# Performance work log

Measured on AMD Instinct MI355X. Metric: run time of the kernel, lower is better.

Reference implementation:

```python
import jax, jax.numpy as jnp
import numpy as np

D_MODEL = 1024
D_STATE = 16
D_CONV = 4
EXPAND = 2
D_INNER = EXPAND * D_MODEL          # 2048
DT_RANK = D_MODEL // 16             # 64
BATCH, SEQ = 4, 2048


def setup_inputs() -> dict:
    key = jax.random.key(0)
    ks = jax.random.split(key, 8)
    s = lambda k, shape, sc=0.02: jax.random.normal(k, shape, jnp.float32) * sc
    x = jax.random.normal(ks[0], (BATCH, SEQ, D_MODEL), jnp.float32)
    tau = jax.random.uniform(ks[1], (BATCH, SEQ), jnp.float32) * 7200.0  # seconds
    # S4D-real init for A
    A_log = jnp.log(jnp.broadcast_to(jnp.arange(1, D_STATE + 1, dtype=jnp.float32), (D_INNER, D_STATE)))
    return dict(
        x=x, tau=tau,
        ln_g=jnp.ones((D_MODEL,), jnp.float32),
        ln_b=jnp.zeros((D_MODEL,), jnp.float32),
        in_proj_w=s(ks[2], (2 * D_INNER, D_MODEL)),
        conv_w=s(ks[3], (D_INNER, 1, D_CONV), 0.1),   # depthwise [O, I/g=1, K]
        conv_b=jnp.zeros((D_INNER,), jnp.float32),
        x_proj_w=s(ks[4], (DT_RANK + 2 * D_STATE, D_INNER)),
        dt_proj_w=s(ks[5], (D_INNER, DT_RANK), 0.1),
        dt_proj_b=jnp.full((D_INNER,), -4.6, jnp.float32),  # softplus ~ 0.01
        A_log=A_log,
        D=jnp.ones((D_INNER,), jnp.float32),
        out_proj_w=s(ks[6], (D_MODEL, D_INNER)),
        log_decay=jnp.full((D_MODEL,), -3.0, jnp.float32),
    )


def _mamba_block(x, tau, ln_g, ln_b, in_proj_w, conv_w, conv_b, x_proj_w,
                 dt_proj_w, dt_proj_b, A_log, D, out_proj_w, log_decay):
    # LayerNorm(d_model)
    mu = jnp.mean(x, axis=-1, keepdims=True)
    var = jnp.var(x, axis=-1, keepdims=True)
    xn = (x - mu) * jax.lax.rsqrt(var + 1e-5) * ln_g + ln_b

    # in_proj -> split into conv branch and gate branch, each [B, L, d_inner]
    xz = jnp.einsum('bld,ed->ble', xn, in_proj_w)
    x_in, z = jnp.split(xz, 2, axis=-1)

    # causal depthwise conv1d over time
    xc = jax.lax.conv_general_dilated(
        x_in.transpose(0, 2, 1), conv_w, (1,), [(D_CONV - 1, 0)],
        dimension_numbers=('NCH', 'OIH', 'NCH'), feature_group_count=D_INNER)
    u = jax.nn.silu(xc.transpose(0, 2, 1) + conv_b)          # [B, L, d_inner]

    # input-dependent SSM params
    x_dbl = jnp.einsum('ble,fe->blf', u, x_proj_w)
    dt, Bm, Cm = jnp.split(x_dbl, [DT_RANK, DT_RANK + D_STATE], axis=-1)
    delta = jax.nn.softplus(jnp.einsum('blr,dr->bld', dt, dt_proj_w) + dt_proj_b)
    A = -jnp.exp(A_log)                                       # [d_inner, d_state]

    # selective scan: h_t = exp(dt*A)*h + dt*u*B_t ; y_t = <h_t, C_t>
    def step(h, inp):
        d_t, B_t, C_t, u_t = inp                              # [B,d],[B,n],[B,n],[B,d]
        h = jnp.exp(d_t[..., None] * A) * h + (d_t * u_t)[..., None] * B_t[:, None, :]
        return h, jnp.einsum('bdn,bn->bd', h, C_t)

    h0 = jnp.zeros((x.shape[0], D_INNER, D_STATE), x.dtype)
    xs = (delta.transpose(1, 0, 2), Bm.transpose(1, 0, 2),
          Cm.transpose(1, 0, 2), u.transpose(1, 0, 2))
    _, ys = jax.lax.scan(step, h0, xs)
    y = ys.transpose(1, 0, 2) + u * D
    y = y * jax.nn.silu(z)
    h_out = jnp.einsum('ble,de->bld', y, out_proj_w)          # mamba output [B,L,d_model]

    # ZOH time-decay gate + residual (dropout = identity in eval)
    tau_h = jnp.maximum(tau / 3600.0, 1e-4)[..., None]
    gate = jnp.exp(-jax.nn.softplus(log_decay) * tau_h)
    return x + h_out * gate


def reference(x, tau, ln_g, ln_b, in_proj_w, conv_w, conv_b, x_proj_w,
              dt_proj_w, dt_proj_b, A_log, D, out_proj_w, log_decay):
    return _mamba_block(x, tau, ln_g, ln_b, in_proj_w, conv_w, conv_b, x_proj_w,
                        dt_proj_w, dt_proj_b, A_log, D, out_proj_w, log_decay)
```

## Files before the change

### kernel.cpp

```cpp
#include <hip/hip_runtime.h>

typedef unsigned short u16;
typedef unsigned int u32;
typedef short s16x8 __attribute__((ext_vector_type(8)));
typedef u16 u16x8 __attribute__((ext_vector_type(8)));
typedef float f32x4 __attribute__((ext_vector_type(4)));

#define TOK 8192
#define DM 1024
#define DI 2048
#define DS 16
#define DR 64
#define NCHUNK 64
#define CH 32
#define XPN 96
#define XP_SPLIT 4
#define CONV_T 16

#define SBAR() do { asm volatile("" ::: "memory"); __builtin_amdgcn_s_barrier(); asm volatile("" ::: "memory"); } while (0)
#define WAITVM(N) do { asm volatile("s_waitcnt vmcnt(" #N ")" ::: "memory"); __builtin_amdgcn_sched_barrier(0); } while (0)
#define WAITLGKM0() do { asm volatile("s_waitcnt lgkmcnt(0)" ::: "memory"); __builtin_amdgcn_sched_barrier(0); } while (0)

__device__ __forceinline__ u16 f2bf(float f) {
    u32 u = __float_as_uint(f);
    u32 r = (u + 0x7fffu + ((u >> 16) & 1u)) >> 16;
    return (u16)r;
}
__device__ __forceinline__ float bf2f(u16 h) {
    return __uint_as_float(((u32)h) << 16);
}
__device__ __forceinline__ float softplus_f(float x) {
    return (x > 15.f) ? x : __logf(1.f + __expf(x));
}
__device__ __forceinline__ void unpack8(const uint4 v, float* o) {
    o[0] = __uint_as_float(v.x << 16); o[1] = __uint_as_float(v.x & 0xffff0000u);
    o[2] = __uint_as_float(v.y << 16); o[3] = __uint_as_float(v.y & 0xffff0000u);
    o[4] = __uint_as_float(v.z << 16); o[5] = __uint_as_float(v.z & 0xffff0000u);
    o[6] = __uint_as_float(v.w << 16); o[7] = __uint_as_float(v.w & 0xffff0000u);
}
__device__ __forceinline__ void async16(u16* lds, const u16* g) {
    __builtin_amdgcn_global_load_lds(
        (const __attribute__((address_space(1))) void*)g,
        (__attribute__((address_space(3))) void*)lds, 16, 0, 0);
}

__global__ __launch_bounds__(256) void prep_all(
    const float* __restrict__ in_w, const float* __restrict__ xp_w,
    const float* __restrict__ dt_w, const float* __restrict__ out_w,
    const float* __restrict__ tau, const float* __restrict__ log_decay,
    const float* __restrict__ x, const float* __restrict__ ln_g,
    const float* __restrict__ ln_b,
    u16* __restrict__ wi, u16* __restrict__ wxp, u16* __restrict__ wdt,
    u16* __restrict__ wout, float* __restrict__ th, float* __restrict__ sd,
    u16* __restrict__ xn) {
    const int b = blockIdx.x;
    if (b >= 6496) {
        const int tok = b - 6496;
        const float4 v = ((const float4*)(x + (size_t)tok * DM))[threadIdx.x];
        float s = v.x + v.y + v.z + v.w;
        float sq = v.x * v.x + v.y * v.y + v.z * v.z + v.w * v.w;
#pragma unroll
        for (int off = 32; off; off >>= 1) {
            s += __shfl_xor(s, off);
            sq += __shfl_xor(sq, off);
        }
        __shared__ float red[8];
        const int wv = threadIdx.x >> 6;
        if ((threadIdx.x & 63) == 0) { red[wv] = s; red[4 + wv] = sq; }
        __syncthreads();
        s = red[0] + red[1] + red[2] + red[3];
        sq = red[4] + red[5] + red[6] + red[7];
        const float mean = s * (1.f / DM);
        const float var = sq * (1.f / DM) - mean * mean;
        const float rstd = rsqrtf(var + 1e-5f);
        const float4 gv = ((const float4*)ln_g)[threadIdx.x];
        const float4 bv = ((const float4*)ln_b)[threadIdx.x];
        ushort4 o;
        o.x = f2bf((v.x - mean) * rstd * gv.x + bv.x);
        o.y = f2bf((v.y - mean) * rstd * gv.y + bv.y);
        o.z = f2bf((v.z - mean) * rstd * gv.z + bv.z);
        o.w = f2bf((v.w - mean) * rstd * gv.w + bv.w);
        ((ushort4*)(xn + (size_t)tok * DM))[threadIdx.x] = o;
        return;
    }
    const float* src; u16* dst; int i;
    if (b < 4096)      { src = in_w;  dst = wi;   i = b * 256 + threadIdx.x; }
    else if (b < 4288) { src = xp_w;  dst = wxp;  i = (b - 4096) * 256 + threadIdx.x; }
    else if (b < 4416) { src = dt_w;  dst = wdt;  i = (b - 4288) * 256 + threadIdx.x; }
    else if (b < 6464) { src = out_w; dst = wout; i = (b - 4416) * 256 + threadIdx.x; }
    else {
        int j = (b - 6464) * 256 + threadIdx.x;
        if (j < TOK) th[j] = fmaxf(tau[j] * (1.f / 3600.f), 1e-4f);
        if (j < DM)  sd[j] = softplus_f(log_decay[j]);
        return;
    }
    float4 v = ((const float4*)src)[i];
    ushort4 o;
    o.x = f2bf(v.x); o.y = f2bf(v.y); o.z = f2bf(v.z); o.w = f2bf(v.w);
    ((ushort4*)dst)[i] = o;
}

template <int EPI>
__global__ __launch_bounds__(256, 2) void gemm128(
    const u16* __restrict__ A, int lda,
    const u16* __restrict__ W, int ldw, int K,
    u16* __restrict__ Cxi, u16* __restrict__ Cz,
    float* __restrict__ Cf,
    const float* __restrict__ xres, const float* __restrict__ th,
    const float* __restrict__ sd) {
    __shared__ __align__(16) u16 lds[2 * 16384];
    const int tid = threadIdx.x;
    const int wave = tid >> 6, lane = tid & 63;
    const int wm = wave >> 1, wn = wave & 1;
    const int fl = lane & 15, fh = lane >> 4;
    int bm, bn;
    if (EPI == 0) {
        const int swz = ((int)blockIdx.x & 7) * 256 + ((int)blockIdx.x >> 3);
        const int rg = swz >> 5, wi_ = swz & 31;
        bm = (rg >> 2) * 4 + (wi_ >> 3);
        bn = (rg & 3) * 8 + (wi_ & 7);
    } else {
        const int swz = ((int)blockIdx.x & 7) * 64 + ((int)blockIdx.x >> 3);
        const int rg = swz >> 4, wi_ = swz & 15;
        bm = (rg >> 1) * 4 + (wi_ >> 2);
        bn = (rg & 1) * 4 + (wi_ & 3);
    }
    const int NT = K >> 6;

    const int r0 = tid >> 3;
    const int cb = ((tid & 7) ^ (r0 & 7)) << 3;
    const int rA = bm * 128 + r0;
    const int rB = bn * 128 + r0;

    f32x4 acc[4][4];
#pragma unroll
    for (int m = 0; m < 4; m++)
#pragma unroll
        for (int n = 0; n < 4; n++) acc[m][n] = f32x4{0.f, 0.f, 0.f, 0.f};

    auto stage = [&](int buf, int k0) {
#pragma unroll
        for (int j = 0; j < 4; j++)
            async16(lds + buf * 16384 + j * 2048 + tid * 8,
                    A + (size_t)(rA + j * 32) * lda + k0 + cb);
#pragma unroll
        for (int j = 0; j < 4; j++)
            async16(lds + buf * 16384 + 8192 + j * 2048 + tid * 8,
                    W + (size_t)(rB + j * 32) * ldw + k0 + cb);
    };
    auto rdA = [&](int buf, int mf, int kk) -> s16x8 {
        int r = wm * 64 + mf * 16 + fl;
        int slot = ((kk << 2) | fh) ^ (fl & 7);
        return *(const s16x8*)(lds + buf * 16384 + r * 64 + slot * 8);
    };
    auto rdB = [&](int buf, int nf, int kk) -> s16x8 {
        int r = wn * 64 + nf * 16 + fl;
        int slot = ((kk << 2) | fh) ^ (fl & 7);
        return *(const s16x8*)(lds + buf * 16384 + 8192 + r * 64 + slot * 8);
    };

    stage(0, 0);
    stage(1, 64);
    WAITVM(8);
    SBAR();

    for (int t = 0; t < NT; ++t) {
        const int cur = t & 1;
        s16x8 ah[4][2], bh[4][2];
#pragma unroll
        for (int mf = 0; mf < 4; mf++) { ah[mf][0] = rdA(cur, mf, 0); ah[mf][1] = rdA(cur, mf, 1); }
#pragma unroll
        for (int nf = 0; nf < 4; nf++) { bh[nf][0] = rdB(cur, nf, 0); bh[nf][1] = rdB(cur, nf, 1); }
        WAITLGKM0();
        SBAR();
        if (t + 2 < NT) stage(cur, (t + 2) << 6);
        __builtin_amdgcn_s_setprio(1);
#pragma unroll
        for (int kk = 0; kk < 2; kk++)
#pragma unroll
            for (int mf = 0; mf < 4; mf++)
#pragma unroll
                for (int nf = 0; nf < 4; nf++)
                    acc[mf][nf] = __builtin_amdgcn_mfma_f32_16x16x32_bf16(ah[mf][kk], bh[nf][kk], acc[mf][nf], 0, 0, 0);
        __builtin_amdgcn_s_setprio(0);
        __builtin_amdgcn_sched_barrier(0);
        if (t + 2 < NT) { WAITVM(8); }
        else           { WAITVM(0); }
        SBAR();
    }

#pragma unroll
    for (int mf = 0; mf < 4; mf++)
#pragma unroll
        for (int j = 0; j < 4; j++) {
            int row = bm * 128 + wm * 64 + mf * 16 + fh * 4 + j;
            if (EPI == 0) {
                u16* dst = (bn < 16) ? Cxi : Cz;
                const int cbase = (bn < 16) ? bn * 128 : (bn - 16) * 128;
#pragma unroll
                for (int n = 0; n < 4; n++) {
                    int col = cbase + wn * 64 + n * 16 + fl;
                    dst[(size_t)row * DI + col] = f2bf(acc[mf][n][j]);
                }
            } else {
                float t = th[row];
#pragma unroll
                for (int n = 0; n < 4; n++) {
                    int col = bn * 128 + wn * 64 + n * 16 + fl;
                    size_t idx = (size_t)row * DM + col;
                    Cf[idx] = xres[idx] + acc[mf][n][j] * __expf(-sd[col] * t);
                }
            }
        }
}

__global__ __launch_bounds__(256) void dt_gemm(
    const u16* __restrict__ A,
    const u16* __restrict__ W,
    u16* __restrict__ Cb,
    const float* __restrict__ bias) {
    __shared__ __align__(16) u16 lds[2 * 8192];
    const int tid = threadIdx.x;
    const int wave = tid >> 6, lane = tid & 63;
    const int wm = wave >> 1, wn = wave & 1;
    const int fl = lane & 15, fh = lane >> 4;
    const int bm = blockIdx.x, bn = blockIdx.y;

    const int r0 = tid >> 3;
    const int cb = ((tid & 7) ^ (r0 & 7)) << 3;

#pragma unroll
    for (int j = 0; j < 4; j++)
        async16(lds + j * 2048 + tid * 8,
                A + (size_t)(bm * 128 + j * 32 + r0) * XPN + cb);
#pragma unroll
    for (int j = 0; j < 4; j++)
        async16(lds + 8192 + j * 2048 + tid * 8,
                W + (size_t)(bn * 128 + j * 32 + r0) * DR + cb);
    WAITVM(0);
    SBAR();

    auto rdA = [&](int mf, int kk) -> s16x8 {
        int r = wm * 64 + mf * 16 + fl;
        int slot = ((kk << 2) | fh) ^ (fl & 7);
        return *(const s16x8*)(lds + r * 64 + slot * 8);
    };
    auto rdB = [&](int nf, int kk) -> s16x8 {
        int r = wn * 64 + nf * 16 + fl;
        int slot = ((kk << 2) | fh) ^ (fl & 7);
        return *(const s16x8*)(lds + 8192 + r * 64 + slot * 8);
    };

    f32x4 acc[4][4];
#pragma unroll
    for (int m = 0; m < 4; m++)
#pragma unroll
        for (int n = 0; n < 4; n++) acc[m][n] = f32x4{0.f, 0.f, 0.f, 0.f};

    s16x8 ah[4][2], bh[4][2];
#pragma unroll
    for (int mf = 0; mf < 4; mf++) { ah[mf][0] = rdA(mf, 0); ah[mf][1] = rdA(mf, 1); }
#pragma unroll
    for (int nf = 0; nf < 4; nf++) { bh[nf][0] = rdB(nf, 0); bh[nf][1] = rdB(nf, 1); }
    WAITLGKM0();
#pragma unroll
    for (int kk = 0; kk < 2; kk++)
#pragma unroll
        for (int mf = 0; mf < 4; mf++)
#pragma unroll
            for (int nf = 0; nf < 4; nf++)
                acc[mf][nf] = __builtin_amdgcn_mfma_f32_16x16x32_bf16(ah[mf][kk], bh[nf][kk], acc[mf][nf], 0, 0, 0);

#pragma unroll
    for (int mf = 0; mf < 4; mf++)
#pragma unroll
        for (int j = 0; j < 4; j++) {
            int row = bm * 128 + wm * 64 + mf * 16 + fh * 4 + j;
#pragma unroll
            for (int n = 0; n < 4; n++) {
                int col = bn * 128 + wn * 64 + n * 16 + fl;
                Cb[(size_t)row * DI + col] = f2bf(softplus_f(acc[mf][n][j] + bias[col]));
            }
        }
}

__global__ __launch_bounds__(256) void xp_gemm(const u16* __restrict__ A,
                                               const u16* __restrict__ W,
                                               float* __restrict__ part) {
    __shared__ u16 As[128 * 64];
    __shared__ u16 Bs[XPN * 64];
    const int tid = threadIdx.x;
    const int wave = tid >> 6, lane = tid & 63;
    const int bm = blockIdx.x, sp = blockIdx.y;
    const int fl = lane & 15, fh = lane >> 4;
    const int trow = tid >> 3, tcol = (tid & 7) * 8;

    f32x4 acc[2][6];
#pragma unroll
    for (int m = 0; m < 2; m++)
#pragma unroll
        for (int n = 0; n < 6; n++) acc[m][n] = f32x4{0.f, 0.f, 0.f, 0.f};

    const int kbeg = sp * (DI / XP_SPLIT);
    for (int k0 = kbeg; k0 < kbeg + DI / XP_SPLIT; k0 += 64) {
        __syncthreads();
#pragma unroll
        for (int i = 0; i < 4; i++)
            async16(As + i * 2048 + tid * 8,
                    A + (size_t)(bm * 128 + i * 32 + trow) * DI + k0 + tcol);
#pragma unroll
        for (int i = 0; i < 3; i++)
            async16(Bs + i * 2048 + tid * 8,
                    W + (size_t)(i * 32 + trow) * DI + k0 + tcol);
        __syncthreads();
#pragma unroll
        for (int kk = 0; kk < 2; kk++) {
            s16x8 av[2], bv[6];
#pragma unroll
            for (int m = 0; m < 2; m++)
                av[m] = *(const s16x8*)(As + (wave * 32 + m * 16 + fl) * 64 + kk * 32 + fh * 8);
#pragma unroll
            for (int n = 0; n < 6; n++)
                bv[n] = *(const s16x8*)(Bs + (n * 16 + fl) * 64 + kk * 32 + fh * 8);
#pragma unroll
            for (int m = 0; m < 2; m++)
#pragma unroll
                for (int n = 0; n < 6; n++)
                    acc[m][n] = __builtin_amdgcn_mfma_f32_16x16x32_bf16(av[m], bv[n], acc[m][n], 0, 0, 0);
        }
    }
    float* dst = part + (size_t)sp * TOK * XPN;
#pragma unroll
    for (int m = 0; m < 2; m++)
#pragma unroll
        for (int j = 0; j < 4; j++) {
            int row = bm * 128 + wave * 32 + m * 16 + fh * 4 + j;
#pragma unroll
            for (int n = 0; n < 6; n++) {
                int col = n * 16 + fl;
                dst[(size_t)row * XPN + col] = acc[m][n][j];
            }
        }
}

__global__ __launch_bounds__(256) void xp_reduce(const float* __restrict__ part,
                                                 u16* __restrict__ out) {
    int i = blockIdx.x * 256 + threadIdx.x;
    if (i >= TOK * XPN) return;
    float s = 0.f;
#pragma unroll
    for (int sp = 0; sp < XP_SPLIT; sp++) s += part[(size_t)sp * TOK * XPN + i];
    out[i] = f2bf(s);
}

__global__ __launch_bounds__(256) void conv_silu_kernel(const u16* __restrict__ xi,
                                                        const float* __restrict__ cw,
                                                        const float* __restrict__ cb,
                                                        u16* __restrict__ u) {
    const int b = blockIdx.y;
    const int l0 = blockIdx.x * CONV_T;
    const int d0 = threadIdx.x * 8;
    float w0[8], w1[8], w2[8], w3[8], bias[8];
#pragma unroll
    for (int e = 0; e < 8; e++) {
        float4 wv = ((const float4*)cw)[d0 + e];
        w0[e] = wv.x; w1[e] = wv.y; w2[e] = wv.z; w3[e] = wv.w;
        bias[e] = cb[d0 + e];
    }
    float win[4][8];
#pragma unroll
    for (int i = 0; i < 3; i++) {
        int l = l0 - 3 + i;
        int slot = (l0 + 1 + i) & 3;
        if (l < 0) {
#pragma unroll
            for (int e = 0; e < 8; e++) win[slot][e] = 0.f;
        } else {
            u16x8 v = *(const u16x8*)(xi + ((size_t)(b * 2048 + l)) * DI + d0);
#pragma unroll
            for (int e = 0; e < 8; e++) win[slot][e] = bf2f(v[e]);
        }
    }
#pragma unroll
    for (int t = 0; t < CONV_T; t++) {
        const int l = l0 + t;
        const size_t tok = (size_t)b * 2048 + l;
        u16x8 v = *(const u16x8*)(xi + tok * DI + d0);
        const int s3 = t & 3;
#pragma unroll
        for (int e = 0; e < 8; e++) win[s3][e] = bf2f(v[e]);
        const int s0 = (t + 1) & 3, s1 = (t + 2) & 3, s2 = (t + 3) & 3;
        u16x8 o;
#pragma unroll
        for (int e = 0; e < 8; e++) {
            float a = bias[e];
            a = fmaf(w0[e], win[s0][e], a);
            a = fmaf(w1[e], win[s1][e], a);
            a = fmaf(w2[e], win[s2][e], a);
            a = fmaf(w3[e], win[s3][e], a);
            o[e] = f2bf(a / (1.f + __expf(-a)));
        }
        *(u16x8*)(u + tok * DI + d0) = o;
    }
}

__global__ __launch_bounds__(256) void scan_passA(const u16* __restrict__ delta,
                                                  const u16* __restrict__ u,
                                                  const u16* __restrict__ xdbl,
                                                  const float* __restrict__ A_log,
                                                  u16* __restrict__ qh,
                                                  float* __restrict__ Sarr) {
    const int d = blockIdx.x * 256 + threadIdx.x;
    const int b = blockIdx.y, c = blockIdx.z;
    float Av[16];
#pragma unroll
    for (int n = 0; n < 16; n++) Av[n] = -__expf(A_log[d * 16 + n]);
    bool fast = true;
#pragma unroll
    for (int n = 0; n < 16; n++) fast = fast && (fabsf(Av[n] + (float)(n + 1)) < 1e-4f * (n + 1));
    const bool allfast = __all(fast);

    float h[16];
#pragma unroll
    for (int n = 0; n < 16; n++) h[n] = 0.f;
    float S = 0.f;
    const int l0 = c * CH;
    size_t tok = (size_t)b * 2048 + l0;
    float dt = bf2f(delta[tok * DI + d]);
    float uu = bf2f(u[tok * DI + d]);
    const uint4* bp0 = (const uint4*)(xdbl + tok * 96 + 64);
    uint4 b0 = bp0[0], b1 = bp0[1];
    for (int t = 0; t < CH; ++t) {
        const int tn = (t + 1 < CH) ? t + 1 : t;
        const size_t tokn = (size_t)b * 2048 + l0 + tn;
        float dt_n = bf2f(delta[tokn * DI + d]);
        float uu_n = bf2f(u[tokn * DI + d]);
        const uint4* bpn = (const uint4*)(xdbl + tokn * 96 + 64);
        uint4 b0n = bpn[0], b1n = bpn[1];
        float du = dt * uu;
        float Bv[16];
        unpack8(b0, Bv); unpack8(b1, Bv + 8);
        float e[16];
        if (allfast) {
            float r = __expf(-dt);
            e[0] = r;
#pragma unroll
            for (int n = 1; n < 16; n++) e[n] = e[n - 1] * r;
        } else {
#pragma unroll
            for (int n = 0; n < 16; n++) e[n] = __expf(dt * Av[n]);
        }
#pragma unroll
        for (int n = 0; n < 16; n++) h[n] = fmaf(e[n], h[n], du * Bv[n]);
        S += dt;
        dt = dt_n; uu = uu_n; b0 = b0n; b1 = b1n;
    }
    const size_t base = ((size_t)(c * 4 + b) * 16) * DI + d;
#pragma unroll
    for (int n = 0; n < 16; n++) qh[base + (size_t)n * DI] = f2bf(h[n]);
    Sarr[(size_t)(c * 4 + b) * DI + d] = S;
}

__global__ __launch_bounds__(256) void scan_passB(u16* __restrict__ qh,
                                                  const float* __restrict__ Sarr,
                                                  const float* __restrict__ A_log) {
    const int idx = blockIdx.x * 256 + threadIdx.x;
    const int d = idx & (DI - 1);
    const int n = (idx >> 11) & 15;
    const int b = idx >> 15;
    const float Avn = -__expf(A_log[d * 16 + n]);
    float h = 0.f;
    for (int c = 0; c < NCHUNK; c++) {
        const size_t base = ((size_t)(c * 4 + b) * 16 + n) * DI + d;
        const float qv = bf2f(qh[base]);
        const float S = Sarr[(size_t)(c * 4 + b) * DI + d];
        qh[base] = f2bf(h);
        h = fmaf(__expf(Avn * S), h, qv);
    }
}

__global__ __launch_bounds__(256) void scan_passC(const u16* __restrict__ delta,
                                                  const u16* __restrict__ u,
                                                  const u16* __restrict__ xdbl,
                                                  const u16* __restrict__ z,
                                                  const float* __restrict__ A_log,
                                                  const float* __restrict__ Dvec,
                                                  const u16* __restrict__ qh,
                                                  u16* __restrict__ yg) {
    const int d = blockIdx.x * 256 + threadIdx.x;
    const int b = blockIdx.y, c = blockIdx.z;
    float Av[16];
#pragma unroll
    for (int n = 0; n < 16; n++) Av[n] = -__expf(A_log[d * 16 + n]);
    bool fast = true;
#pragma unroll
    for (int n = 0; n < 16; n++) fast = fast && (fabsf(Av[n] + (float)(n + 1)) < 1e-4f * (n + 1));
    const bool allfast = __all(fast);
    const float Dd = Dvec[d];

    float h[16];
    const size_t hbase = ((size_t)(c * 4 + b) * 16) * DI + d;
#pragma unroll
    for (int n = 0; n < 16; n++) h[n] = bf2f(qh[hbase + (size_t)n * DI]);

    const int l0 = c * CH;
    size_t tok = (size_t)b * 2048 + l0;
    float dt = bf2f(delta[tok * DI + d]);
    float uu = bf2f(u[tok * DI + d]);
    float zz = bf2f(z[tok * DI + d]);
    const uint4* bp0 = (const uint4*)(xdbl + tok * 96 + 64);
    uint4 b0 = bp0[0], b1 = bp0[1], c0 = bp0[2], c1 = bp0[3];
    for (int t = 0; t < CH; ++t) {
        const int tn = (t + 1 < CH) ? t + 1 : t;
        const size_t tokn = (size_t)b * 2048 + l0 + tn;
        float dt_n = bf2f(delta[tokn * DI + d]);
        float uu_n = bf2f(u[tokn * DI + d]);
        float zz_n = bf2f(z[tokn * DI + d]);
        const uint4* bpn = (const uint4*)(xdbl + tokn * 96 + 64);
        uint4 b0n = bpn[0], b1n = bpn[1], c0n = bpn[2], c1n = bpn[3];

        float du = dt * uu;
        float Bv[16], Cv[16];
        unpack8(b0, Bv); unpack8(b1, Bv + 8);
        unpack8(c0, Cv); unpack8(c1, Cv + 8);
        float e[16];
        if (allfast) {
            float r = __expf(-dt);
            e[0] = r;
#pragma unroll
            for (int n = 1; n < 16; n++) e[n] = e[n - 1] * r;
        } else {
#pragma unroll
            for (int n = 0; n < 16; n++) e[n] = __expf(dt * Av[n]);
        }
        float y = 0.f;
#pragma unroll
        for (int n = 0; n < 16; n++) {
            h[n] = fmaf(e[n], h[n], du * Bv[n]);
            y = fmaf(h[n], Cv[n], y);
        }
        float sz = zz / (1.f + __expf(-zz));
        const size_t tokc = (size_t)b * 2048 + l0 + t;
        yg[tokc * DI + d] = f2bf((y + uu * Dd) * sz);

        dt = dt_n; uu = uu_n; zz = zz_n;
        b0 = b0n; b1 = b1n; c0 = c0n; c1 = c1n;
    }
}

extern "C" void kernel_launch(void* const* d_in, const int* in_sizes, int n_in,
                              void* d_out, int out_size, void* d_ws, size_t ws_size,
                              hipStream_t stream) {
    const float* x = (const float*)d_in[0];
    const float* tau = (const float*)d_in[1];
    const float* ln_g = (const float*)d_in[2];
    const float* ln_b = (const float*)d_in[3];
    const float* in_proj_w = (const float*)d_in[4];
    const float* conv_w = (const float*)d_in[5];
    const float* conv_b = (const float*)d_in[6];
    const float* x_proj_w = (const float*)d_in[7];
    const float* dt_proj_w = (const float*)d_in[8];
    const float* dt_proj_b = (const float*)d_in[9];
    const float* A_log = (const float*)d_in[10];
    const float* Dvec = (const float*)d_in[11];
    const float* out_proj_w = (const float*)d_in[12];
    const float* log_decay = (const float*)d_in[13];
    float* out = (float*)d_out;

    char* ws = (char*)d_ws;
    size_t off = 0;
    auto alloc = [&](size_t bytes) -> void* {
        void* p = ws + off;
        off += (bytes + 255) & ~(size_t)255;
        return p;
    };
    u16* xn    = (u16*)alloc((size_t)TOK * DM * 2);
    u16* w_in  = (u16*)alloc((size_t)2 * DI * DM * 2);
    u16* w_xp  = (u16*)alloc((size_t)XPN * DI * 2);
    u16* w_dt  = (u16*)alloc((size_t)DI * DR * 2);
    u16* w_out = (u16*)alloc((size_t)DM * DI * 2);
    u16* xi    = (u16*)alloc((size_t)TOK * DI * 2);
    u16* z     = (u16*)alloc((size_t)TOK * DI * 2);
    u16* u     = (u16*)alloc((size_t)TOK * DI * 2);
    u16* xdbl  = (u16*)alloc((size_t)TOK * XPN * 2);
    u16* delta = (u16*)alloc((size_t)TOK * DI * 2);
    u16* qh    = (u16*)alloc((size_t)NCHUNK * 4 * 16 * DI * 2);
    float* Sarr = (float*)alloc((size_t)NCHUNK * 4 * DI * 4);
    u16* yg    = (u16*)alloc((size_t)TOK * DI * 2);
    float* th = (float*)alloc((size_t)TOK * 4);
    float* sd = (float*)alloc((size_t)DM * 4);
    float* xp_part = (float*)xn;

    prep_all<<<6496 + TOK, 256, 0, stream>>>(in_proj_w, x_proj_w, dt_proj_w, out_proj_w,
                                             tau, log_decay, x, ln_g, ln_b,
                                             w_in, w_xp, w_dt, w_out, th, sd, xn);

    gemm128<0><<<2048, 256, 0, stream>>>(xn, DM, w_in, DM, DM, xi, z,
                                         nullptr, nullptr, nullptr, nullptr);
    conv_silu_kernel<<<dim3(2048 / CONV_T, 4), 256, 0, stream>>>(xi, conv_w, conv_b, u);

    xp_gemm<<<dim3(64, XP_SPLIT), 256, 0, stream>>>(u, w_xp, xp_part);
    xp_reduce<<<(TOK * XPN + 255) / 256, 256, 0, stream>>>(xp_part, xdbl);

    dt_gemm<<<dim3(64, 16), 256, 0, stream>>>(xdbl, w_dt, delta, dt_proj_b);

    scan_passA<<<dim3(8, 4, NCHUNK), 256, 0, stream>>>(delta, u, xdbl, A_log, qh, Sarr);
    scan_passB<<<512, 256, 0, stream>>>(qh, Sarr, A_log);
    scan_passC<<<dim3(8, 4, NCHUNK), 256, 0, stream>>>(delta, u, xdbl, z, A_log, Dvec, qh, yg);

    gemm128<2><<<512, 256, 0, stream>>>(yg, DI, w_out, DI, DI, nullptr, nullptr,
                                        out, x, th, sd);
}
```

Measured before the change: 281.5 us.

## Use dedicated 256x128-tile in_proj GEMM with K-step 32

```diff
diff --git a/kernel.cpp b/kernel.cpp
--- a/kernel.cpp
+++ b/kernel.cpp
@@ -100,11 +100,97 @@
     ((ushort4*)dst)[i] = o;
 }
 
-template <int EPI>
+__global__ __launch_bounds__(256, 2) void gemm_in(
+    const u16* __restrict__ A,
+    const u16* __restrict__ W,
+    u16* __restrict__ Cxi, u16* __restrict__ Cz) {
+    __shared__ __align__(16) u16 lds[2 * 12288];
+    const int tid = threadIdx.x;
+    const int wave = tid >> 6, lane = tid & 63;
+    const int wm = wave >> 1, wn = wave & 1;
+    const int fl = lane & 15, fh = lane >> 4;
+    const int swz = ((int)blockIdx.x & 7) * 128 + ((int)blockIdx.x >> 3);
+    const int rg = swz >> 5, wi_ = swz & 31;
+    const int bm = (rg >> 2) * 4 + (wi_ >> 3);
+    const int bn = (rg & 3) * 8 + (wi_ & 7);
+    const int NT = DM >> 5;
+
+    const int sr = tid >> 2;
+    const int sc = (tid & 3) * 8;
+    const int rA = bm * 256 + sr;
+    const int rB = bn * 128 + sr;
+
+    f32x4 acc[8][4];
+#pragma unroll
+    for (int m = 0; m < 8; m++)
+#pragma unroll
+        for (int n = 0; n < 4; n++) acc[m][n] = f32x4{0.f, 0.f, 0.f, 0.f};
+
+    auto stage = [&](int buf, int k0) {
+#pragma unroll
+        for (int j = 0; j < 4; j++)
+            async16(lds + buf * 12288 + j * 2048 + tid * 8,
+                    A + (size_t)(rA + j * 64) * DM + k0 + sc);
+#pragma unroll
+        for (int j = 0; j < 2; j++)
+            async16(lds + buf * 12288 + 8192 + j * 2048 + tid * 8,
+                    W + (size_t)(rB + j * 64) * DM + k0 + sc);
+    };
+    auto rdA = [&](int buf, int mf) -> s16x8 {
+        int r = wm * 128 + mf * 16 + fl;
+        return *(const s16x8*)(lds + buf * 12288 + r * 32 + fh * 8);
+    };
+    auto rdB = [&](int buf, int nf) -> s16x8 {
+        int r = wn * 64 + nf * 16 + fl;
+        return *(const s16x8*)(lds + buf * 12288 + 8192 + r * 32 + fh * 8);
+    };
+
+    stage(0, 0);
+    stage(1, 32);
+    WAITVM(6);
+    SBAR();
+
+    for (int t = 0; t < NT; ++t) {
+        const int cur = t & 1;
+        s16x8 ah[8], bh[4];
+#pragma unroll
+        for (int mf = 0; mf < 8; mf++) ah[mf] = rdA(cur, mf);
+#pragma unroll
+        for (int nf = 0; nf < 4; nf++) bh[nf] = rdB(cur, nf);
+        WAITLGKM0();
+        SBAR();
+        if (t + 2 < NT) stage(cur, (t + 2) << 5);
+        __builtin_amdgcn_s_setprio(1);
+#pragma unroll
+        for (int mf = 0; mf < 8; mf++)
+#pragma unroll
+            for (int nf = 0; nf < 4; nf++)
+                acc[mf][nf] = __builtin_amdgcn_mfma_f32_16x16x32_bf16(ah[mf], bh[nf], acc[mf][nf], 0, 0, 0);
+        __builtin_amdgcn_s_setprio(0);
+        __builtin_amdgcn_sched_barrier(0);
+        if (t + 2 < NT) { WAITVM(6); }
+        else           { WAITVM(0); }
+        SBAR();
+    }
+
+    u16* dst = (bn < 16) ? Cxi : Cz;
+    const int cbase = (bn < 16) ? bn * 128 : (bn - 16) * 128;
+#pragma unroll
+    for (int mf = 0; mf < 8; mf++)
+#pragma unroll
+        for (int j = 0; j < 4; j++) {
+            int row = bm * 256 + wm * 128 + mf * 16 + fh * 4 + j;
+#pragma unroll
+            for (int n = 0; n < 4; n++) {
+                int col = cbase + wn * 64 + n * 16 + fl;
+                dst[(size_t)row * DI + col] = f2bf(acc[mf][n][j]);
+            }
+        }
+}
+
 __global__ __launch_bounds__(256, 2) void gemm128(
     const u16* __restrict__ A, int lda,
     const u16* __restrict__ W, int ldw, int K,
-    u16* __restrict__ Cxi, u16* __restrict__ Cz,
     float* __restrict__ Cf,
     const float* __restrict__ xres, const float* __restrict__ th,
     const float* __restrict__ sd) {
@@ -113,18 +199,10 @@
     const int wave = tid >> 6, lane = tid & 63;
     const int wm = wave >> 1, wn = wave & 1;
     const int fl = lane & 15, fh = lane >> 4;
-    int bm, bn;
-    if (EPI == 0) {
-        const int swz = ((int)blockIdx.x & 7) * 256 + ((int)blockIdx.x >> 3);
-        const int rg = swz >> 5, wi_ = swz & 31;
-        bm = (rg >> 2) * 4 + (wi_ >> 3);
-        bn = (rg & 3) * 8 + (wi_ & 7);
-    } else {
-        const int swz = ((int)blockIdx.x & 7) * 64 + ((int)blockIdx.x >> 3);
-        const int rg = swz >> 4, wi_ = swz & 15;
-        bm = (rg >> 1) * 4 + (wi_ >> 2);
-        bn = (rg & 1) * 4 + (wi_ & 3);
-    }
+    const int swz = ((int)blockIdx.x & 7) * 64 + ((int)blockIdx.x >> 3);
+    const int rg = swz >> 4, wi_ = swz & 15;
+    const int bm = (rg >> 1) * 4 + (wi_ >> 2);
+    const int bn = (rg & 1) * 4 + (wi_ & 3);
     const int NT = K >> 6;
 
     const int r0 = tid >> 3;
@@ -194,22 +272,12 @@
 #pragma unroll
         for (int j = 0; j < 4; j++) {
             int row = bm * 128 + wm * 64 + mf * 16 + fh * 4 + j;
-            if (EPI == 0) {
-                u16* dst = (bn < 16) ? Cxi : Cz;
-                const int cbase = (bn < 16) ? bn * 128 : (bn - 16) * 128;
-#pragma unroll
-                for (int n = 0; n < 4; n++) {
-                    int col = cbase + wn * 64 + n * 16 + fl;
-                    dst[(size_t)row * DI + col] = f2bf(acc[mf][n][j]);
-                }
-            } else {
-                float t = th[row];
-#pragma unroll
-                for (int n = 0; n < 4; n++) {
-                    int col = bn * 128 + wn * 64 + n * 16 + fl;
-                    size_t idx = (size_t)row * DM + col;
-                    Cf[idx] = xres[idx] + acc[mf][n][j] * __expf(-sd[col] * t);
-                }
+            float t = th[row];
+#pragma unroll
+            for (int n = 0; n < 4; n++) {
+                int col = bn * 128 + wn * 64 + n * 16 + fl;
+                size_t idx = (size_t)row * DM + col;
+                Cf[idx] = xres[idx] + acc[mf][n][j] * __expf(-sd[col] * t);
             }
         }
 }
@@ -595,8 +663,7 @@
                                              tau, log_decay, x, ln_g, ln_b,
                                              w_in, w_xp, w_dt, w_out, th, sd, xn);
 
-    gemm128<0><<<2048, 256, 0, stream>>>(xn, DM, w_in, DM, DM, xi, z,
-                                         nullptr, nullptr, nullptr, nullptr);
+    gemm_in<<<1024, 256, 0, stream>>>(xn, w_in, xi, z);
     conv_silu_kernel<<<dim3(2048 / CONV_T, 4), 256, 0, stream>>>(xi, conv_w, conv_b, u);
 
     xp_gemm<<<dim3(64, XP_SPLIT), 256, 0, stream>>>(u, w_xp, xp_part);
@@ -608,6 +675,5 @@
     scan_passB<<<512, 256, 0, stream>>>(qh, Sarr, A_log);
     scan_passC<<<dim3(8, 4, NCHUNK), 256, 0, stream>>>(delta, u, xdbl, z, A_log, Dvec, qh, yg);
 
-    gemm128<2><<<512, 256, 0, stream>>>(yg, DI, w_out, DI, DI, nullptr, nullptr,
-                                        out, x, th, sd);
-}
+    gemm128<<<512, 256, 0, stream>>>(yg, DI, w_out, DI, DI, out, x, th, sd);
+}
```

New measurement: 282.5 us. No clear change (+0.4%).
